# Optimization experiments

Hardware: AMD Instinct MI355X
Metric: run time of the kernel (lower is better)

The kernel has to match this reference:

```python
import jax, jax.numpy as jnp
import numpy as np

B, T, DIM, HID = 8, 2048, 1024, 128

def setup_inputs() -> dict:
    key = jax.random.key(0)
    ks = jax.random.split(key, 6)
    x = jax.random.normal(ks[0], (B, T, DIM), dtype=jnp.float32)
    wk_w = jax.random.normal(ks[1], (DIM, HID), dtype=jnp.float32) * 0.02
    wk_b = jnp.zeros((HID,), dtype=jnp.float32)
    wv_w = jax.random.normal(ks[2], (DIM, HID), dtype=jnp.float32) * 0.02
    wv_b = jnp.zeros((HID,), dtype=jnp.float32)
    # xavier_uniform for w [T,T]: bound = sqrt(6/(T+T))
    bound = float(np.sqrt(6.0 / (T + T)))
    w = jax.random.uniform(ks[3], (T, T), dtype=jnp.float32, minval=-bound, maxval=bound)
    return {"x": x, "wk_w": wk_w, "wk_b": wk_b, "wv_w": wv_w, "wv_b": wv_b, "w": w}

def reference(x, wk_w, wk_b, wv_w, wv_b, w):
    # K, V projections: [B,T,HID]
    K = x @ wk_w + wk_b
    V = x @ wv_w + wv_b
    eK = jnp.exp(K)            # [B,T,HID]
    ew = jnp.exp(w)            # [T,T], shared left operand of both matmuls
    num = jnp.einsum('ts,bsh->bth', ew, eK * V)  # exp(w) @ (exp(K)*V)
    den = jnp.einsum('ts,bsh->bth', ew, eK)      # exp(w) @ exp(K)
    # Original module returns `weighted` (before sigmoid(Q) gating and ffnn)
    return num / den
```

## Files before the change

kernel.cpp:

```cpp
#include <hip/hip_runtime.h>
#include <hip/hip_bf16.h>


#define T_    2048
#define DIM_  1024
#define HID_  128

typedef __attribute__((ext_vector_type(8))) __bf16 bf16x8;
typedef __attribute__((ext_vector_type(4))) float f32x4;
typedef __attribute__((ext_vector_type(4))) unsigned short us4;
typedef __attribute__((ext_vector_type(8))) unsigned short us8;

typedef const unsigned int __attribute__((address_space(1)))* gas_t;
typedef unsigned int __attribute__((address_space(3)))* las_t;

__device__ __forceinline__ unsigned short f2bf(float f) {
    unsigned int u = __builtin_bit_cast(unsigned int, f);
    u += 0x7fffu + ((u >> 16) & 1u);
    return (unsigned short)(u >> 16);
}

__device__ __forceinline__ void gload16(const void* g, void* l) {
    __builtin_amdgcn_global_load_lds((gas_t)g, (las_t)l, 16, 0, 0);
}

__global__ __launch_bounds__(256) void prep_ew(const float* __restrict__ w,
                                               unsigned short* __restrict__ ew) {
    int idx = blockIdx.x * 256 + threadIdx.x;
    f32x4 v = ((const f32x4*)w)[idx];
    us4 o;
    o[0] = f2bf(__expf(v[0]));
    o[1] = f2bf(__expf(v[1]));
    o[2] = f2bf(__expf(v[2]));
    o[3] = f2bf(__expf(v[3]));
    ((us4*)ew)[idx] = o;
}

__global__ __launch_bounds__(256) void prep_wkv(const float* __restrict__ wk,
                                                const float* __restrict__ wv,
                                                unsigned short* __restrict__ wkvT) {
    int t = blockIdx.x * 256 + threadIdx.x;
    int n = t & 255, k = t >> 8;
    float v = (n < 128) ? wk[k * 128 + n] : wv[k * 128 + (n - 128)];
    wkvT[n * 1024 + k] = f2bf(v);
}

__global__ __launch_bounds__(256) void gemm1(const float* __restrict__ x,
                                             const unsigned short* __restrict__ wkvT,
                                             const float* __restrict__ wk_b,
                                             const float* __restrict__ wv_b,
                                             unsigned short* __restrict__ KVc) {
    __shared__ __align__(16) unsigned short As[32 * 72];
    __shared__ __align__(16) unsigned short Bs[256 * 64];
    const int tid  = threadIdx.x;
    const int m0   = blockIdx.x * 32;
    const int bb   = m0 >> 11;
    const int t0   = m0 & (T_ - 1);
    const int wave = tid >> 6, lane = tid & 63;
    const int lr = lane & 15, lq = lane >> 4;

    f32x4 acc[2][4];
#pragma unroll
    for (int i = 0; i < 2; i++)
#pragma unroll
        for (int j = 0; j < 4; j++) acc[i][j] = {0.f, 0.f, 0.f, 0.f};

    for (int t = 0; t < 16; t++) {
        int k0 = t * 64;
        __syncthreads();
#pragma unroll
        for (int i = 0; i < 8; i++) {
            int c = i * 256 + tid, r = c >> 3, kc = ((c & 7) ^ (r & 7)) * 8;
            gload16(wkvT + (size_t)r * DIM_ + k0 + kc, &Bs[(i * 256 + wave * 64) * 8]);
        }
        f32x4 areg[2];
#pragma unroll
        for (int i = 0; i < 2; i++) {
            int c = i * 256 + tid, r = c >> 4, c4 = (c & 15) * 4;
            areg[i] = *(const f32x4*)(x + (size_t)(m0 + r) * DIM_ + k0 + c4);
        }
#pragma unroll
        for (int i = 0; i < 2; i++) {
            int c = i * 256 + tid, r = c >> 4, c4 = (c & 15) * 4;
            us4 o;
            o[0] = f2bf(areg[i][0]); o[1] = f2bf(areg[i][1]);
            o[2] = f2bf(areg[i][2]); o[3] = f2bf(areg[i][3]);
            *(us4*)(&As[r * 72 + c4]) = o;
        }
        __syncthreads();
#pragma unroll
        for (int ks = 0; ks < 64; ks += 32) {
            bf16x8 af[2], bfr[4];
#pragma unroll
            for (int mf = 0; mf < 2; mf++)
                af[mf] = *(const bf16x8*)(&As[(mf * 16 + lr) * 72 + ks + lq * 8]);
#pragma unroll
            for (int nf = 0; nf < 4; nf++) {
                int rb = (nf < 2) ? (wave * 32 + nf * 16 + lr)
                                  : (128 + wave * 32 + (nf - 2) * 16 + lr);
                bfr[nf] = *(const bf16x8*)(&Bs[rb * 64 + ((ks + lq * 8) ^ ((rb & 7) << 3))]);
            }
#pragma unroll
            for (int mf = 0; mf < 2; mf++)
#pragma unroll
                for (int nf = 0; nf < 4; nf++)
                    acc[mf][nf] = __builtin_amdgcn_mfma_f32_16x16x32_bf16(
                        af[mf], bfr[nf], acc[mf][nf], 0, 0, 0);
        }
    }

    __syncthreads();
    unsigned short* ekvS = &Bs[0];
    unsigned short* ekS  = ekvS + 128 * 40;
#pragma unroll
    for (int nf = 0; nf < 2; nf++) {
        int h = wave * 32 + nf * 16 + lr;
        float bk = wk_b[h], bv = wv_b[h];
#pragma unroll
        for (int mf = 0; mf < 2; mf++) {
            int m = mf * 16 + lq * 4;
            us4 ok, okv;
#pragma unroll
            for (int j = 0; j < 4; j++) {
                float ek = __expf(acc[mf][nf][j] + bk);
                float vv = acc[mf][nf + 2][j] + bv;
                ok[j]  = f2bf(ek);
                okv[j] = f2bf(ek * vv);
            }
            *(us4*)(ekS  + h * 40 + m) = ok;
            *(us4*)(ekvS + h * 40 + m) = okv;
        }
    }
    __syncthreads();
    unsigned short* dst = KVc + (size_t)bb * 256 * T_;
#pragma unroll
    for (int i = 0; i < 2; i++) {
        int c = i * 256 + tid;
        int h = c >> 2, mc = (c & 3) * 8;
        us8 vkv = *(const us8*)(ekvS + h * 40 + mc);
        us8 vk  = *(const us8*)(ekS  + h * 40 + mc);
        *(us8*)(dst + (size_t)h * T_ + t0 + mc)         = vkv;
        *(us8*)(dst + (size_t)(128 + h) * T_ + t0 + mc) = vk;
    }
}

__global__ __launch_bounds__(256) void gemm2(const unsigned short* __restrict__ ew,
                                             const unsigned short* __restrict__ KVc,
                                             float* __restrict__ out) {
    __shared__ __align__(16) unsigned short As[32 * 64];
    __shared__ __align__(16) unsigned short Bs[256 * 64];
    const int tid  = threadIdx.x;
    const int t0   = blockIdx.x * 32;
    const int b    = blockIdx.y;
    const unsigned short* Bsrc = KVc + (size_t)b * 256 * T_;
    const int wave = tid >> 6, lane = tid & 63;
    const int lr = lane & 15, lq = lane >> 4;

    f32x4 acc[2][4];
#pragma unroll
    for (int i = 0; i < 2; i++)
#pragma unroll
        for (int j = 0; j < 4; j++) acc[i][j] = {0.f, 0.f, 0.f, 0.f};

    for (int t = 0; t < 32; t++) {
        int k0 = t * 64;
        __syncthreads();
        {
            int c = tid, r = c >> 3, kc = ((c & 7) ^ (r & 7)) * 8;
            gload16(ew + (size_t)(t0 + r) * T_ + k0 + kc, &As[(wave * 64) * 8]);
        }
#pragma unroll
        for (int i = 0; i < 8; i++) {
            int c = i * 256 + tid, r = c >> 3, kc = ((c & 7) ^ (r & 7)) * 8;
            gload16(Bsrc + (size_t)r * T_ + k0 + kc, &Bs[(i * 256 + wave * 64) * 8]);
        }
        __syncthreads();
#pragma unroll
        for (int ks = 0; ks < 64; ks += 32) {
            bf16x8 af[2], bfr[4];
#pragma unroll
            for (int mf = 0; mf < 2; mf++) {
                int ra = mf * 16 + lr;
                af[mf] = *(const bf16x8*)(&As[ra * 64 + ((ks + lq * 8) ^ ((ra & 7) << 3))]);
            }
#pragma unroll
            for (int nf = 0; nf < 4; nf++) {
                int rb = (nf < 2) ? (wave * 32 + nf * 16 + lr)
                                  : (128 + wave * 32 + (nf - 2) * 16 + lr);
                bfr[nf] = *(const bf16x8*)(&Bs[rb * 64 + ((ks + lq * 8) ^ ((rb & 7) << 3))]);
            }
#pragma unroll
            for (int mf = 0; mf < 2; mf++)
#pragma unroll
                for (int nf = 0; nf < 4; nf++)
                    acc[mf][nf] = __builtin_amdgcn_mfma_f32_16x16x32_bf16(
                        af[mf], bfr[nf], acc[mf][nf], 0, 0, 0);
        }
    }

    float* ob = out + ((size_t)b * T_ + t0) * HID_;
#pragma unroll
    for (int nf = 0; nf < 2; nf++) {
        int h = wave * 32 + nf * 16 + lr;
#pragma unroll
        for (int mf = 0; mf < 2; mf++) {
            int m = mf * 16 + lq * 4;
#pragma unroll
            for (int j = 0; j < 4; j++)
                ob[(size_t)(m + j) * HID_ + h] = acc[mf][nf][j] / acc[mf][nf + 2][j];
        }
    }
}

extern "C" void kernel_launch(void* const* d_in, const int* in_sizes, int n_in,
                              void* d_out, int out_size, void* d_ws, size_t ws_size,
                              hipStream_t stream) {
    const float* x    = (const float*)d_in[0];
    const float* wk_w = (const float*)d_in[1];
    const float* wk_b = (const float*)d_in[2];
    const float* wv_w = (const float*)d_in[3];
    const float* wv_b = (const float*)d_in[4];
    const float* w    = (const float*)d_in[5];

    char* ws = (char*)d_ws;
    unsigned short* ws_ew   = (unsigned short*)(ws);
    unsigned short* ws_wkvT = (unsigned short*)(ws + (8u << 20));
    unsigned short* ws_KVc  = (unsigned short*)(ws + (9u << 20));

    prep_ew  <<<4096, 256, 0, stream>>>(w, ws_ew);
    prep_wkv <<<1024, 256, 0, stream>>>(wk_w, wv_w, ws_wkvT);
    gemm1    <<<512, 256, 0, stream>>>(x, ws_wkvT, wk_b, wv_b, ws_KVc);
    gemm2    <<<dim3(64, 8), 256, 0, stream>>>(ws_ew, ws_KVc, (float*)d_out);
}
```

Before: 168.0 us.

## Double-buffer LDS tiles in both GEMMs and vectorize weight transpose

Both GEMM kernels now use two LDS buffers, issuing the async global-to-LDS loads for the next K tile before computing on the current one. Manual vmcnt waits and raw barriers replace the full syncthreads pair, so load latency can overlap the MFMA work. The weight transpose kernel now has each thread produce eight contiguous bf16 values with one 16-byte store, using fewer blocks. Doubling LDS per block (about 73 KB in gemm2) may lower occupancy, and the hand-set vmcnt counts must match the number of loads the compiler actually emits.

```diff
diff --git a/kernel.cpp b/kernel.cpp
--- a/kernel.cpp
+++ b/kernel.cpp
@@ -40,9 +40,12 @@
                                                 const float* __restrict__ wv,
                                                 unsigned short* __restrict__ wkvT) {
     int t = blockIdx.x * 256 + threadIdx.x;
-    int n = t & 255, k = t >> 8;
-    float v = (n < 128) ? wk[k * 128 + n] : wv[k * 128 + (n - 128)];
-    wkvT[n * 1024 + k] = f2bf(v);
+    int n = t & 255, k0 = (t >> 8) << 3;
+    const float* src = (n < 128) ? (wk + n) : (wv + (n - 128));
+    us8 o;
+#pragma unroll
+    for (int j = 0; j < 8; j++) o[j] = f2bf(src[(size_t)(k0 + j) * 128]);
+    *(us8*)(&wkvT[n * 1024 + k0]) = o;
 }
 
 __global__ __launch_bounds__(256) void gemm1(const float* __restrict__ x,
@@ -50,8 +53,8 @@
                                              const float* __restrict__ wk_b,
                                              const float* __restrict__ wv_b,
                                              unsigned short* __restrict__ KVc) {
-    __shared__ __align__(16) unsigned short As[32 * 72];
-    __shared__ __align__(16) unsigned short Bs[256 * 64];
+    __shared__ __align__(16) unsigned short As[2][32 * 72];
+    __shared__ __align__(16) unsigned short Bs[2][256 * 64];
     const int tid  = threadIdx.x;
     const int m0   = blockIdx.x * 32;
     const int bb   = m0 >> 11;
@@ -65,40 +68,58 @@
 #pragma unroll
         for (int j = 0; j < 4; j++) acc[i][j] = {0.f, 0.f, 0.f, 0.f};
 
+    f32x4 aC[2], aN[2];
+#pragma unroll
+    for (int i = 0; i < 2; i++) {
+        int c = i * 256 + tid, r = c >> 4, c4 = (c & 15) * 4;
+        aC[i] = *(const f32x4*)(x + (size_t)(m0 + r) * DIM_ + c4);
+    }
+#pragma unroll
+    for (int i = 0; i < 8; i++) {
+        int c = i * 256 + tid, r = c >> 3, kc = ((c & 7) ^ (r & 7)) * 8;
+        gload16(wkvT + (size_t)r * DIM_ + kc, &Bs[0][(i * 256 + wave * 64) * 8]);
+    }
+
+    int cur = 0;
     for (int t = 0; t < 16; t++) {
-        int k0 = t * 64;
-        __syncthreads();
-#pragma unroll
-        for (int i = 0; i < 8; i++) {
-            int c = i * 256 + tid, r = c >> 3, kc = ((c & 7) ^ (r & 7)) * 8;
-            gload16(wkvT + (size_t)r * DIM_ + k0 + kc, &Bs[(i * 256 + wave * 64) * 8]);
-        }
-        f32x4 areg[2];
-#pragma unroll
-        for (int i = 0; i < 2; i++) {
-            int c = i * 256 + tid, r = c >> 4, c4 = (c & 15) * 4;
-            areg[i] = *(const f32x4*)(x + (size_t)(m0 + r) * DIM_ + k0 + c4);
+        if (t < 15) {
+            int k0 = (t + 1) * 64;
+#pragma unroll
+            for (int i = 0; i < 2; i++) {
+                int c = i * 256 + tid, r = c >> 4, c4 = (c & 15) * 4;
+                aN[i] = *(const f32x4*)(x + (size_t)(m0 + r) * DIM_ + k0 + c4);
+            }
+#pragma unroll
+            for (int i = 0; i < 8; i++) {
+                int c = i * 256 + tid, r = c >> 3, kc = ((c & 7) ^ (r & 7)) * 8;
+                gload16(wkvT + (size_t)r * DIM_ + k0 + kc,
+                        &Bs[cur ^ 1][(i * 256 + wave * 64) * 8]);
+            }
+            asm volatile("s_waitcnt vmcnt(10)" ::: "memory");
+        } else {
+            asm volatile("s_waitcnt vmcnt(0)" ::: "memory");
         }
 #pragma unroll
         for (int i = 0; i < 2; i++) {
             int c = i * 256 + tid, r = c >> 4, c4 = (c & 15) * 4;
             us4 o;
-            o[0] = f2bf(areg[i][0]); o[1] = f2bf(areg[i][1]);
-            o[2] = f2bf(areg[i][2]); o[3] = f2bf(areg[i][3]);
-            *(us4*)(&As[r * 72 + c4]) = o;
-        }
-        __syncthreads();
+            o[0] = f2bf(aC[i][0]); o[1] = f2bf(aC[i][1]);
+            o[2] = f2bf(aC[i][2]); o[3] = f2bf(aC[i][3]);
+            *(us4*)(&As[cur][r * 72 + c4]) = o;
+        }
+        asm volatile("s_waitcnt lgkmcnt(0)" ::: "memory");
+        __builtin_amdgcn_s_barrier();
 #pragma unroll
         for (int ks = 0; ks < 64; ks += 32) {
             bf16x8 af[2], bfr[4];
 #pragma unroll
             for (int mf = 0; mf < 2; mf++)
-                af[mf] = *(const bf16x8*)(&As[(mf * 16 + lr) * 72 + ks + lq * 8]);
+                af[mf] = *(const bf16x8*)(&As[cur][(mf * 16 + lr) * 72 + ks + lq * 8]);
 #pragma unroll
             for (int nf = 0; nf < 4; nf++) {
                 int rb = (nf < 2) ? (wave * 32 + nf * 16 + lr)
                                   : (128 + wave * 32 + (nf - 2) * 16 + lr);
-                bfr[nf] = *(const bf16x8*)(&Bs[rb * 64 + ((ks + lq * 8) ^ ((rb & 7) << 3))]);
+                bfr[nf] = *(const bf16x8*)(&Bs[cur][rb * 64 + ((ks + lq * 8) ^ ((rb & 7) << 3))]);
             }
 #pragma unroll
             for (int mf = 0; mf < 2; mf++)
@@ -107,10 +128,12 @@
                     acc[mf][nf] = __builtin_amdgcn_mfma_f32_16x16x32_bf16(
                         af[mf], bfr[nf], acc[mf][nf], 0, 0, 0);
         }
-    }
-
-    __syncthreads();
-    unsigned short* ekvS = &Bs[0];
+        __builtin_amdgcn_s_barrier();
+        aC[0] = aN[0]; aC[1] = aN[1];
+        cur ^= 1;
+    }
+
+    unsigned short* ekvS = &Bs[0][0];
     unsigned short* ekS  = ekvS + 128 * 40;
 #pragma unroll
     for (int nf = 0; nf < 2; nf++) {
@@ -147,8 +170,8 @@
 __global__ __launch_bounds__(256) void gemm2(const unsigned short* __restrict__ ew,
                                              const unsigned short* __restrict__ KVc,
                                              float* __restrict__ out) {
-    __shared__ __align__(16) unsigned short As[32 * 64];
-    __shared__ __align__(16) unsigned short Bs[256 * 64];
+    __shared__ __align__(16) unsigned short As[2][32 * 64];
+    __shared__ __align__(16) unsigned short Bs[2][256 * 64];
     const int tid  = threadIdx.x;
     const int t0   = blockIdx.x * 32;
     const int b    = blockIdx.y;
@@ -162,32 +185,40 @@
 #pragma unroll
         for (int j = 0; j < 4; j++) acc[i][j] = {0.f, 0.f, 0.f, 0.f};
 
+#define STAGE2(BUF, K0) do {                                                      \
+    { int c = tid, r = c >> 3, kc = ((c & 7) ^ (r & 7)) * 8;                      \
+      gload16(ew + (size_t)(t0 + r) * T_ + (K0) + kc, &As[BUF][(wave * 64) * 8]); } \
+    _Pragma("unroll")                                                             \
+    for (int i = 0; i < 8; i++) {                                                 \
+        int c = i * 256 + tid, r = c >> 3, kc = ((c & 7) ^ (r & 7)) * 8;          \
+        gload16(Bsrc + (size_t)r * T_ + (K0) + kc,                                \
+                &Bs[BUF][(i * 256 + wave * 64) * 8]);                             \
+    } } while (0)
+
+    STAGE2(0, 0);
+
+    int cur = 0;
     for (int t = 0; t < 32; t++) {
-        int k0 = t * 64;
-        __syncthreads();
-        {
-            int c = tid, r = c >> 3, kc = ((c & 7) ^ (r & 7)) * 8;
-            gload16(ew + (size_t)(t0 + r) * T_ + k0 + kc, &As[(wave * 64) * 8]);
-        }
-#pragma unroll
-        for (int i = 0; i < 8; i++) {
-            int c = i * 256 + tid, r = c >> 3, kc = ((c & 7) ^ (r & 7)) * 8;
-            gload16(Bsrc + (size_t)r * T_ + k0 + kc, &Bs[(i * 256 + wave * 64) * 8]);
-        }
-        __syncthreads();
+        if (t < 31) {
+            STAGE2(cur ^ 1, (t + 1) * 64);
+            asm volatile("s_waitcnt vmcnt(9)" ::: "memory");
+        } else {
+            asm volatile("s_waitcnt vmcnt(0)" ::: "memory");
+        }
+        __builtin_amdgcn_s_barrier();
 #pragma unroll
         for (int ks = 0; ks < 64; ks += 32) {
             bf16x8 af[2], bfr[4];
 #pragma unroll
             for (int mf = 0; mf < 2; mf++) {
                 int ra = mf * 16 + lr;
-                af[mf] = *(const bf16x8*)(&As[ra * 64 + ((ks + lq * 8) ^ ((ra & 7) << 3))]);
+                af[mf] = *(const bf16x8*)(&As[cur][ra * 64 + ((ks + lq * 8) ^ ((ra & 7) << 3))]);
             }
 #pragma unroll
             for (int nf = 0; nf < 4; nf++) {
                 int rb = (nf < 2) ? (wave * 32 + nf * 16 + lr)
                                   : (128 + wave * 32 + (nf - 2) * 16 + lr);
-                bfr[nf] = *(const bf16x8*)(&Bs[rb * 64 + ((ks + lq * 8) ^ ((rb & 7) << 3))]);
+                bfr[nf] = *(const bf16x8*)(&Bs[cur][rb * 64 + ((ks + lq * 8) ^ ((rb & 7) << 3))]);
             }
 #pragma unroll
             for (int mf = 0; mf < 2; mf++)
@@ -196,7 +227,10 @@
                     acc[mf][nf] = __builtin_amdgcn_mfma_f32_16x16x32_bf16(
                         af[mf], bfr[nf], acc[mf][nf], 0, 0, 0);
         }
-    }
+        __builtin_amdgcn_s_barrier();
+        cur ^= 1;
+    }
+#undef STAGE2
 
     float* ob = out + ((size_t)b * T_ + t0) * HID_;
 #pragma unroll
@@ -228,7 +262,7 @@
     unsigned short* ws_KVc  = (unsigned short*)(ws + (9u << 20));
 
     prep_ew  <<<4096, 256, 0, stream>>>(w, ws_ew);
-    prep_wkv <<<1024, 256, 0, stream>>>(wk_w, wv_w, ws_wkvT);
-    gemm1    <<<512, 256, 0, stream>>>(x, ws_wkvT, wk_b, wv_b, ws_KVc);
+    prep_wkv <<<128,  256, 0, stream>>>(wk_w, wv_w, ws_wkvT);
+    gemm1    <<<512,  256, 0, stream>>>(x, ws_wkvT, wk_b, wv_b, ws_KVc);
     gemm2    <<<dim3(64, 8), 256, 0, stream>>>(ws_ew, ws_KVc, (float*)d_out);
 }
```

After: 165.6 us. About the same (-1.4%).
